# Optimization experiments

Measured on AMD Instinct MI355X. Metric: run time of the kernel, lower is better.

Reference implementation:

```python
import jax, jax.numpy as jnp
import numpy as np

WINDOW_SIZE = 11
SIGMA = 1.5
C1 = 0.01 ** 2
C2 = 0.03 ** 2


def _gaussian_window(window_size=WINDOW_SIZE, sigma=SIGMA):
    coords = jnp.arange(window_size, dtype=jnp.float32) - window_size // 2
    g = jnp.exp(-(coords ** 2) / (2.0 * sigma ** 2))
    g = g / g.sum()
    w3d = g[:, None, None] * g[None, :, None] * g[None, None, :]
    w3d = w3d / w3d.sum()
    return w3d[None, None]  # [1, 1, K, K, K] (OIDHW)


def _gconv3d(x, window):
    # depthwise 3D conv, SAME padding (pad = K//2), groups = C
    C = x.shape[1]
    w = jnp.broadcast_to(window, (C, 1) + window.shape[2:])
    pad = window.shape[-1] // 2
    return jax.lax.conv_general_dilated(
        x, w,
        window_strides=(1, 1, 1),
        padding=[(pad, pad)] * 3,
        dimension_numbers=("NCDHW", "OIDHW", "NCDHW"),
        feature_group_count=C,
    )


def setup_inputs() -> dict:
    key = jax.random.key(0)
    k1, k2 = jax.random.split(key)
    shape = (4, 1, 64, 192, 192)  # [B, C, D, H, W]
    pred = jax.random.uniform(k1, shape, dtype=jnp.float32)
    target = jax.random.uniform(k2, shape, dtype=jnp.float32)
    return {"pred": pred, "target": target}


def reference(pred, target):
    window = _gaussian_window()
    mu_p = _gconv3d(pred, window)
    mu_t = _gconv3d(target, window)
    mu_p_sq = mu_p ** 2
    mu_t_sq = mu_t ** 2
    mu_pt = mu_p * mu_t
    sigma_p_sq = _gconv3d(pred ** 2, window) - mu_p_sq
    sigma_t_sq = _gconv3d(target ** 2, window) - mu_t_sq
    sigma_pt = _gconv3d(pred * target, window) - mu_pt
    ssim_map = ((2.0 * mu_pt + C1) * (2.0 * sigma_pt + C2)) / (
        (mu_p_sq + mu_t_sq + C1) * (sigma_p_sq + sigma_t_sq + C2)
    )
    return 1.0 - ssim_map.mean()
```

## Files before the change

### kernel.cpp

```cpp
#include <hip/hip_runtime.h>


#define D_DIM 64
#define H_DIM 192
#define W_DIM 192
#define SLICE (H_DIM * W_DIM)
#define VOL   (D_DIM * SLICE)
#define NB    4
#define KS    11
#define RAD   5
#define TH    32
#define TW    48
#define HT    (TH + 2 * RAD)
#define WTT   (TW + 2 * RAD)
#define SPITCH 59
#define IP2   48
#define IPF2  (HT * IP2)
#define C1F   (0.01f * 0.01f)
#define C2F   (0.03f * 0.03f)

typedef _Float16 h2v __attribute__((ext_vector_type(2)));

__device__ __forceinline__ void make_window(float* g) {
    float s = 0.f;
#pragma unroll
    for (int i = 0; i < KS; ++i) {
        float c = (float)(i - RAD);
        g[i] = expf(-(c * c) * (1.0f / 4.5f));
        s += g[i];
    }
    float inv = 1.0f / s;
#pragma unroll
    for (int i = 0; i < KS; ++i) g[i] *= inv;
}

__global__ __launch_bounds__(256) void hw_blur_kernel(
    const float* __restrict__ pred, const float* __restrict__ targ,
    uint2* __restrict__ Xg, unsigned short* __restrict__ Yg, int b0) {
    __shared__ union U {
        float stage[2 * HT * SPITCH];
        unsigned short obuf[5 * TH * TW];
    } u;
    __shared__ _Float16 interm2[5 * IPF2];
    float* sp = u.stage;
    float* st = u.stage + HT * SPITCH;

    float g[KS];
    make_window(g);

    const int tid = threadIdx.x;
    const int d    = blockIdx.y;
    const int tile = blockIdx.x;
    const int h0 = (tile >> 2) * TH;
    const int w0 = (tile & 3) * TW;
    const int bl = blockIdx.z;

    const int in_base = (b0 + bl) * VOL + d * SLICE;

    for (int i = tid; i < HT * SPITCH; i += 256) {
        int y = i / SPITCH, x = i - y * SPITCH;
        int gh = h0 + y - RAD, gw = w0 + x - RAD;
        float pv = 0.f, tv = 0.f;
        if (x < WTT && (unsigned)gh < (unsigned)H_DIM && (unsigned)gw < (unsigned)W_DIM) {
            int idx = in_base + gh * W_DIM + gw;
            pv = pred[idx];
            tv = targ[idx];
        }
        sp[i] = pv;
        st[i] = tv;
    }
    __syncthreads();

    if (tid < 252) {
        const int y = tid / 6;
        const int x0 = (tid % 6) * 8;
        float wp[18], wt[18];
#pragma unroll
        for (int k = 0; k < 18; ++k) {
            wp[k] = sp[y * SPITCH + x0 + k];
            wt[k] = st[y * SPITCH + x0 + k];
        }
#pragma unroll
        for (int o = 0; o < 8; ++o) {
            float s0 = 0.f, s1 = 0.f, s2 = 0.f, s3 = 0.f, s4 = 0.f;
#pragma unroll
            for (int k = 0; k < KS; ++k) {
                float pv = wp[o + k], tv = wt[o + k], gk = g[k];
                s0 += gk * pv;
                s1 += gk * tv;
                s2 += gk * pv * pv;
                s3 += gk * tv * tv;
                s4 += gk * pv * tv;
            }
            int idx = y * IP2 + x0 + o;
            interm2[0 * IPF2 + idx] = (_Float16)s0;
            interm2[1 * IPF2 + idx] = (_Float16)s1;
            interm2[2 * IPF2 + idx] = (_Float16)s2;
            interm2[3 * IPF2 + idx] = (_Float16)s3;
            interm2[4 * IPF2 + idx] = (_Float16)s4;
        }
    }
    __syncthreads();

    if (tid < 240) {
        const int f = tid / TW;
        const int x = tid % TW;
        const _Float16* col = interm2 + f * IPF2 + x;
        unsigned short* ob = u.obuf + f * (TH * TW) + x;
        float acc[KS];
#pragma unroll
        for (int s = 0; s < KS; ++s) acc[s] = 0.f;
#pragma unroll
        for (int yy = 0; yy < HT; ++yy) {
            float v = (float)col[yy * IP2];
#pragma unroll
            for (int m = 0; m < KS; ++m) {
                if (yy < 10 && m < 10 - yy) continue;
                acc[(yy + m + 1) % KS] += g[10 - m] * v;
            }
            if (yy >= 10) {
                const int y = yy - 10;
                const int s = (yy + 1) % KS;
                _Float16 h = (_Float16)acc[s];
                ob[y * TW] = *(unsigned short*)&h;
                acc[s] = 0.f;
            }
        }
    }
    __syncthreads();

    const size_t pl_base = (size_t)(bl * D_DIM + d) * SLICE;
#pragma unroll
    for (int it = 0; it < 6; ++it) {
        int px = it * 256 + tid;
        int y = px / TW, x = px - y * TW;
        unsigned a0 = u.obuf[0 * (TH * TW) + px];
        unsigned a1 = u.obuf[1 * (TH * TW) + px];
        unsigned a2 = u.obuf[2 * (TH * TW) + px];
        unsigned a3 = u.obuf[3 * (TH * TW) + px];
        unsigned a4 = u.obuf[4 * (TH * TW) + px];
        size_t gi = pl_base + (size_t)(h0 + y) * W_DIM + (w0 + x);
        Xg[gi] = make_uint2(a0 | (a1 << 16), a2 | (a3 << 16));
        Yg[gi] = (unsigned short)a4;
    }
}


#define LOADP(s, q) do {                                                  \
    const int _o = (q) * SLICE;                                           \
    uint2 _r = xg[_o];                                                    \
    h2v _l = __builtin_bit_cast(h2v, _r.x);                               \
    h2v _h = __builtin_bit_cast(h2v, _r.y);                               \
    w0[s] = (float)_l[0]; w1[s] = (float)_l[1];                           \
    w2[s] = (float)_h[0]; w3[s] = (float)_h[1];                           \
    w4[s] = (float)__builtin_bit_cast(_Float16, (unsigned short)yg[(q) * SLICE]); \
} while (0)

#define PRE(i, q) do {                                                    \
    xr##i = xg[(q) * SLICE];                                              \
    yr##i = yg[(q) * SLICE];                                              \
} while (0)

#define CMT(s, i) do {                                                    \
    h2v _l = __builtin_bit_cast(h2v, xr##i.x);                            \
    h2v _h = __builtin_bit_cast(h2v, xr##i.y);                            \
    w0[s] = (float)_l[0]; w1[s] = (float)_l[1];                           \
    w2[s] = (float)_h[0]; w3[s] = (float)_h[1];                           \
    w4[s] = (float)__builtin_bit_cast(_Float16, (unsigned short)yr##i);   \
} while (0)

#define SSIM_ACC(MP, MT, E2, T2, PT) do {                                 \
    float _mps = (MP) * (MP), _mts = (MT) * (MT), _mpt = (MP) * (MT);     \
    float _num = (2.f * _mpt + C1F) * (2.f * ((PT) - _mpt) + C2F);        \
    float _den = (_mps + _mts + C1F) *                                    \
                 (((E2) - _mps) + ((T2) - _mts) + C2F);                   \
    ssim_sum += _num * __builtin_amdgcn_rcpf(_den);                       \
} while (0)

#define EMIT_W(r, JHI) do {                                               \
    float _mp = 0.f, _mt = 0.f, _e2 = 0.f, _t2 = 0.f, _pt = 0.f;          \
    _Pragma("unroll")                                                     \
    for (int _j = 0; _j <= (JHI); ++_j) {                                 \
        const int _s = (1 + (r) + _j) % 11; const float _g = g[_j];       \
        _mp += _g * w0[_s]; _mt += _g * w1[_s]; _e2 += _g * w2[_s];       \
        _t2 += _g * w3[_s]; _pt += _g * w4[_s];                           \
    }                                                                     \
    SSIM_ACC(_mp, _mt, _e2, _t2, _pt);                                    \
} while (0)

#define EMIT_IN(d) do {                                                   \
    float _mp = 0.f, _mt = 0.f, _e2 = 0.f, _t2 = 0.f, _pt = 0.f;          \
    _Pragma("unroll")                                                     \
    for (int _j = 5 - (d); _j < 11; ++_j) {                               \
        const int _s = (d) - 5 + _j; const float _g = g[_j];              \
        _mp += _g * w0[_s]; _mt += _g * w1[_s]; _e2 += _g * w2[_s];       \
        _t2 += _g * w3[_s]; _pt += _g * w4[_s];                           \
    }                                                                     \
    SSIM_ACC(_mp, _mt, _e2, _t2, _pt);                                    \
} while (0)

#define RND(r, i, qn)  do { CMT(r, i); PRE(i, qn); EMIT_W(r, 10); } while (0)
#define RNDL(r, i)     do { CMT(r, i); EMIT_W(r, 10); } while (0)

__global__ __launch_bounds__(256) void dblur_ssim_kernel(
    const uint2* __restrict__ Xg, const unsigned short* __restrict__ Yg,
    float* __restrict__ partials) {
    float g[KS];
    make_window(g);

    const int tid = threadIdx.x;
    const int bl = blockIdx.x / 144;
    const int hw = (blockIdx.x % 144) * 256 + tid;
    const int cb = bl * VOL + hw;
    const uint2* xg = Xg + cb;
    const unsigned short* yg = Yg + cb;

    float w0[KS], w1[KS], w2[KS], w3[KS], w4[KS];
    uint2 xr0, xr1, xr2, xr3;
    unsigned yr0, yr1, yr2, yr3;
    float ssim_sum = 0.f;

    if (blockIdx.y == 0) {
        LOADP(0, 0); LOADP(1, 1); LOADP(2, 2); LOADP(3, 3); LOADP(4, 4);
        LOADP(5, 5); LOADP(6, 6); LOADP(7, 7); LOADP(8, 8); LOADP(9, 9);
        LOADP(10, 10);
        PRE(3, 11); PRE(0, 12); PRE(1, 13); PRE(2, 14);
        EMIT_IN(0); EMIT_IN(1); EMIT_IN(2); EMIT_IN(3); EMIT_IN(4); EMIT_IN(5);
        RND(0, 3, 15);  RND(1, 0, 16);  RND(2, 1, 17);  RND(3, 2, 18);
        RND(4, 3, 19);  RND(5, 0, 20);  RND(6, 1, 21);  RND(7, 2, 22);
        RND(8, 3, 23);  RND(9, 0, 24);  RND(10, 1, 25); RND(0, 2, 26);
        RND(1, 3, 27);  RND(2, 0, 28);  RND(3, 1, 29);  RND(4, 2, 30);
        RND(5, 3, 31);  RND(6, 0, 32);  RND(7, 1, 33);  RND(8, 2, 34);
        RND(9, 3, 35);  RND(10, 0, 36);
        RNDL(0, 1); RNDL(1, 2); RNDL(2, 3); RNDL(3, 0);
    } else {
        LOADP(5, 27); LOADP(6, 28); LOADP(7, 29); LOADP(8, 30); LOADP(9, 31);
        LOADP(10, 32); LOADP(0, 33); LOADP(1, 34); LOADP(2, 35); LOADP(3, 36);
        LOADP(4, 37);
        PRE(2, 38); PRE(3, 39); PRE(0, 40); PRE(1, 41);
        EMIT_W(4, 10);
        RND(5, 2, 42);  RND(6, 3, 43);  RND(7, 0, 44);  RND(8, 1, 45);
        RND(9, 2, 46);  RND(10, 3, 47); RND(0, 0, 48);  RND(1, 1, 49);
        RND(2, 2, 50);  RND(3, 3, 51);  RND(4, 0, 52);  RND(5, 1, 53);
        RND(6, 2, 54);  RND(7, 3, 55);  RND(8, 0, 56);  RND(9, 1, 57);
        RND(10, 2, 58); RND(0, 3, 59);  RND(1, 0, 60);  RND(2, 1, 61);
        RND(3, 2, 62);  RND(4, 3, 63);
        RNDL(5, 0); RNDL(6, 1); RNDL(7, 2); RNDL(8, 3);
        EMIT_W(9, 9); EMIT_W(10, 8); EMIT_W(11, 7); EMIT_W(12, 6); EMIT_W(13, 5);
    }

    float a = ssim_sum;
#pragma unroll
    for (int off = 32; off > 0; off >>= 1) a += __shfl_down(a, off, 64);
    __shared__ float red[4];
    int lane = tid & 63, wv = tid >> 6;
    if (lane == 0) red[wv] = a;
    __syncthreads();
    if (tid == 0)
        partials[blockIdx.y * gridDim.x + blockIdx.x] =
            red[0] + red[1] + red[2] + red[3];
}

__global__ __launch_bounds__(256) void finalize_kernel(
    const float* __restrict__ partials, int n, float* __restrict__ out) {
    double a = 0.0;
    for (int i = threadIdx.x; i < n; i += 256) a += (double)partials[i];
#pragma unroll
    for (int off = 32; off > 0; off >>= 1) a += __shfl_down(a, off, 64);
    __shared__ double red[4];
    int lane = threadIdx.x & 63, wv = threadIdx.x >> 6;
    if (lane == 0) red[wv] = a;
    __syncthreads();
    if (threadIdx.x == 0) {
        double s = red[0] + red[1] + red[2] + red[3];
        out[0] = (float)(1.0 - s / (double)((long long)NB * VOL));
    }
}

extern "C" void kernel_launch(void* const* d_in, const int* in_sizes, int n_in,
                              void* d_out, int out_size, void* d_ws, size_t ws_size,
                              hipStream_t stream) {
    const float* pred = (const float*)d_in[0];
    const float* targ = (const float*)d_in[1];
    float* out = (float*)d_out;

    int G = 4;
    while (G > 1 && (size_t)G * VOL * 10 + 8192 > ws_size) G >>= 1;

    uint2* Xg = (uint2*)d_ws;
    unsigned short* Yg = (unsigned short*)((char*)d_ws + (size_t)G * VOL * 8);
    float* partials = (float*)((char*)d_ws + (size_t)G * VOL * 10);
    const int bpc = G * 144;
    const int nchunks = NB / G;

    for (int c = 0; c < nchunks; ++c) {
        hw_blur_kernel<<<dim3(24, D_DIM, G), 256, 0, stream>>>(
            pred, targ, Xg, Yg, c * G);
        dblur_ssim_kernel<<<dim3(bpc, 2), 256, 0, stream>>>(
            Xg, Yg, partials + c * 2 * bpc);
    }
    finalize_kernel<<<1, 256, 0, stream>>>(partials, NB * 288, out);
}
```

Before: 212.9 us.

## Fuse HW and depth blur into single streaming SSIM kernel

Replaces the two-kernel pipeline, which wrote five fp16 blurred planes to global workspace and read them back, with one kernel. Each block owns a 16x16 HW tile and marches through depth, blurring each slice in LDS and accumulating the depth blur in rolling register accumulators. It prefetches the next slice into registers while the current one is computed. This removes the large intermediate global write and read, at the cost of halo re-reads, per-slice barriers and higher register pressure.

```diff
diff --git a/kernel.cpp b/kernel.cpp
--- a/kernel.cpp
+++ b/kernel.cpp
@@ -9,13 +9,10 @@
 #define NB    4
 #define KS    11
 #define RAD   5
-#define TH    32
-#define TW    48
-#define HT    (TH + 2 * RAD)
-#define WTT   (TW + 2 * RAD)
-#define SPITCH 59
-#define IP2   48
-#define IPF2  (HT * IP2)
+#define TIL   16
+#define HLO   26
+#define SP    48
+#define IPX   6
 #define C1F   (0.01f * 0.01f)
 #define C2F   (0.03f * 0.03f)
 
@@ -33,141 +30,6 @@
 #pragma unroll
     for (int i = 0; i < KS; ++i) g[i] *= inv;
 }
-
-__global__ __launch_bounds__(256) void hw_blur_kernel(
-    const float* __restrict__ pred, const float* __restrict__ targ,
-    uint2* __restrict__ Xg, unsigned short* __restrict__ Yg, int b0) {
-    __shared__ union U {
-        float stage[2 * HT * SPITCH];
-        unsigned short obuf[5 * TH * TW];
-    } u;
-    __shared__ _Float16 interm2[5 * IPF2];
-    float* sp = u.stage;
-    float* st = u.stage + HT * SPITCH;
-
-    float g[KS];
-    make_window(g);
-
-    const int tid = threadIdx.x;
-    const int d    = blockIdx.y;
-    const int tile = blockIdx.x;
-    const int h0 = (tile >> 2) * TH;
-    const int w0 = (tile & 3) * TW;
-    const int bl = blockIdx.z;
-
-    const int in_base = (b0 + bl) * VOL + d * SLICE;
-
-    for (int i = tid; i < HT * SPITCH; i += 256) {
-        int y = i / SPITCH, x = i - y * SPITCH;
-        int gh = h0 + y - RAD, gw = w0 + x - RAD;
-        float pv = 0.f, tv = 0.f;
-        if (x < WTT && (unsigned)gh < (unsigned)H_DIM && (unsigned)gw < (unsigned)W_DIM) {
-            int idx = in_base + gh * W_DIM + gw;
-            pv = pred[idx];
-            tv = targ[idx];
-        }
-        sp[i] = pv;
-        st[i] = tv;
-    }
-    __syncthreads();
-
-    if (tid < 252) {
-        const int y = tid / 6;
-        const int x0 = (tid % 6) * 8;
-        float wp[18], wt[18];
-#pragma unroll
-        for (int k = 0; k < 18; ++k) {
-            wp[k] = sp[y * SPITCH + x0 + k];
-            wt[k] = st[y * SPITCH + x0 + k];
-        }
-#pragma unroll
-        for (int o = 0; o < 8; ++o) {
-            float s0 = 0.f, s1 = 0.f, s2 = 0.f, s3 = 0.f, s4 = 0.f;
-#pragma unroll
-            for (int k = 0; k < KS; ++k) {
-                float pv = wp[o + k], tv = wt[o + k], gk = g[k];
-                s0 += gk * pv;
-                s1 += gk * tv;
-                s2 += gk * pv * pv;
-                s3 += gk * tv * tv;
-                s4 += gk * pv * tv;
-            }
-            int idx = y * IP2 + x0 + o;
-            interm2[0 * IPF2 + idx] = (_Float16)s0;
-            interm2[1 * IPF2 + idx] = (_Float16)s1;
-            interm2[2 * IPF2 + idx] = (_Float16)s2;
-            interm2[3 * IPF2 + idx] = (_Float16)s3;
-            interm2[4 * IPF2 + idx] = (_Float16)s4;
-        }
-    }
-    __syncthreads();
-
-    if (tid < 240) {
-        const int f = tid / TW;
-        const int x = tid % TW;
-        const _Float16* col = interm2 + f * IPF2 + x;
-        unsigned short* ob = u.obuf + f * (TH * TW) + x;
-        float acc[KS];
-#pragma unroll
-        for (int s = 0; s < KS; ++s) acc[s] = 0.f;
-#pragma unroll
-        for (int yy = 0; yy < HT; ++yy) {
-            float v = (float)col[yy * IP2];
-#pragma unroll
-            for (int m = 0; m < KS; ++m) {
-                if (yy < 10 && m < 10 - yy) continue;
-                acc[(yy + m + 1) % KS] += g[10 - m] * v;
-            }
-            if (yy >= 10) {
-                const int y = yy - 10;
-                const int s = (yy + 1) % KS;
-                _Float16 h = (_Float16)acc[s];
-                ob[y * TW] = *(unsigned short*)&h;
-                acc[s] = 0.f;
-            }
-        }
-    }
-    __syncthreads();
-
-    const size_t pl_base = (size_t)(bl * D_DIM + d) * SLICE;
-#pragma unroll
-    for (int it = 0; it < 6; ++it) {
-        int px = it * 256 + tid;
-        int y = px / TW, x = px - y * TW;
-        unsigned a0 = u.obuf[0 * (TH * TW) + px];
-        unsigned a1 = u.obuf[1 * (TH * TW) + px];
-        unsigned a2 = u.obuf[2 * (TH * TW) + px];
-        unsigned a3 = u.obuf[3 * (TH * TW) + px];
-        unsigned a4 = u.obuf[4 * (TH * TW) + px];
-        size_t gi = pl_base + (size_t)(h0 + y) * W_DIM + (w0 + x);
-        Xg[gi] = make_uint2(a0 | (a1 << 16), a2 | (a3 << 16));
-        Yg[gi] = (unsigned short)a4;
-    }
-}
-
-
-#define LOADP(s, q) do {                                                  \
-    const int _o = (q) * SLICE;                                           \
-    uint2 _r = xg[_o];                                                    \
-    h2v _l = __builtin_bit_cast(h2v, _r.x);                               \
-    h2v _h = __builtin_bit_cast(h2v, _r.y);                               \
-    w0[s] = (float)_l[0]; w1[s] = (float)_l[1];                           \
-    w2[s] = (float)_h[0]; w3[s] = (float)_h[1];                           \
-    w4[s] = (float)__builtin_bit_cast(_Float16, (unsigned short)yg[(q) * SLICE]); \
-} while (0)
-
-#define PRE(i, q) do {                                                    \
-    xr##i = xg[(q) * SLICE];                                              \
-    yr##i = yg[(q) * SLICE];                                              \
-} while (0)
-
-#define CMT(s, i) do {                                                    \
-    h2v _l = __builtin_bit_cast(h2v, xr##i.x);                            \
-    h2v _h = __builtin_bit_cast(h2v, xr##i.y);                            \
-    w0[s] = (float)_l[0]; w1[s] = (float)_l[1];                           \
-    w2[s] = (float)_h[0]; w3[s] = (float)_h[1];                           \
-    w4[s] = (float)__builtin_bit_cast(_Float16, (unsigned short)yr##i);   \
-} while (0)
 
 #define SSIM_ACC(MP, MT, E2, T2, PT) do {                                 \
     float _mps = (MP) * (MP), _mts = (MT) * (MT), _mpt = (MP) * (MT);     \
@@ -177,87 +39,152 @@
     ssim_sum += _num * __builtin_amdgcn_rcpf(_den);                       \
 } while (0)
 
-#define EMIT_W(r, JHI) do {                                               \
-    float _mp = 0.f, _mt = 0.f, _e2 = 0.f, _t2 = 0.f, _pt = 0.f;          \
-    _Pragma("unroll")                                                     \
-    for (int _j = 0; _j <= (JHI); ++_j) {                                 \
-        const int _s = (1 + (r) + _j) % 11; const float _g = g[_j];       \
-        _mp += _g * w0[_s]; _mt += _g * w1[_s]; _e2 += _g * w2[_s];       \
-        _t2 += _g * w3[_s]; _pt += _g * w4[_s];                           \
-    }                                                                     \
-    SSIM_ACC(_mp, _mt, _e2, _t2, _pt);                                    \
-} while (0)
-
-#define EMIT_IN(d) do {                                                   \
-    float _mp = 0.f, _mt = 0.f, _e2 = 0.f, _t2 = 0.f, _pt = 0.f;          \
-    _Pragma("unroll")                                                     \
-    for (int _j = 5 - (d); _j < 11; ++_j) {                               \
-        const int _s = (d) - 5 + _j; const float _g = g[_j];              \
-        _mp += _g * w0[_s]; _mt += _g * w1[_s]; _e2 += _g * w2[_s];       \
-        _t2 += _g * w3[_s]; _pt += _g * w4[_s];                           \
-    }                                                                     \
-    SSIM_ACC(_mp, _mt, _e2, _t2, _pt);                                    \
-} while (0)
-
-#define RND(r, i, qn)  do { CMT(r, i); PRE(i, qn); EMIT_W(r, 10); } while (0)
-#define RNDL(r, i)     do { CMT(r, i); EMIT_W(r, 10); } while (0)
-
-__global__ __launch_bounds__(256) void dblur_ssim_kernel(
-    const uint2* __restrict__ Xg, const unsigned short* __restrict__ Yg,
+__global__ __launch_bounds__(256) void fused_ssim_kernel(
+    const float* __restrict__ pred, const float* __restrict__ targ,
     float* __restrict__ partials) {
+    __shared__ float spb[HLO * SP];
+    __shared__ float stb[HLO * SP];
+    __shared__ __attribute__((aligned(16))) _Float16 interm[HLO * TIL * IPX];
+    __shared__ float red[4];
+
     float g[KS];
     make_window(g);
 
     const int tid = threadIdx.x;
-    const int bl = blockIdx.x / 144;
-    const int hw = (blockIdx.x % 144) * 256 + tid;
-    const int cb = bl * VOL + hw;
-    const uint2* xg = Xg + cb;
-    const unsigned short* yg = Yg + cb;
-
-    float w0[KS], w1[KS], w2[KS], w3[KS], w4[KS];
-    uint2 xr0, xr1, xr2, xr3;
-    unsigned yr0, yr1, yr2, yr3;
+    const int h0 = (blockIdx.x / 12) * TIL;
+    const int w0 = (blockIdx.x % 12) * TIL;
+    const int half = blockIdx.y;
+    const float* pb = pred + (size_t)blockIdx.z * VOL;
+    const float* tb = targ + (size_t)blockIdx.z * VOL;
+    const int q0 = half ? 27 : 0;
+    const int q1 = half ? 63 : 36;
+    const int d_lo = half ? 32 : 0;
+    const int d_hi = half ? 63 : 31;
+
+    int sidx[3], slds[3];
+    bool sa[3], sv[3];
+#pragma unroll
+    for (int k = 0; k < 3; ++k) {
+        int i = tid + 256 * k;
+        sa[k] = i < HLO * HLO;
+        int y = i / HLO, x = i - y * HLO;
+        int gh = h0 + y - RAD, gw = w0 + x - RAD;
+        sv[k] = sa[k] && (unsigned)gh < (unsigned)H_DIM &&
+                (unsigned)gw < (unsigned)W_DIM;
+        sidx[k] = gh * W_DIM + gw;
+        slds[k] = y * SP + x;
+    }
+    const int py = tid >> 4, px = tid & 15;
+
+    float a0[KS], a1[KS], a2[KS], a3[KS], a4[KS];
+#pragma unroll
+    for (int j = 0; j < KS; ++j)
+        a0[j] = a1[j] = a2[j] = a3[j] = a4[j] = 0.f;
     float ssim_sum = 0.f;
 
-    if (blockIdx.y == 0) {
-        LOADP(0, 0); LOADP(1, 1); LOADP(2, 2); LOADP(3, 3); LOADP(4, 4);
-        LOADP(5, 5); LOADP(6, 6); LOADP(7, 7); LOADP(8, 8); LOADP(9, 9);
-        LOADP(10, 10);
-        PRE(3, 11); PRE(0, 12); PRE(1, 13); PRE(2, 14);
-        EMIT_IN(0); EMIT_IN(1); EMIT_IN(2); EMIT_IN(3); EMIT_IN(4); EMIT_IN(5);
-        RND(0, 3, 15);  RND(1, 0, 16);  RND(2, 1, 17);  RND(3, 2, 18);
-        RND(4, 3, 19);  RND(5, 0, 20);  RND(6, 1, 21);  RND(7, 2, 22);
-        RND(8, 3, 23);  RND(9, 0, 24);  RND(10, 1, 25); RND(0, 2, 26);
-        RND(1, 3, 27);  RND(2, 0, 28);  RND(3, 1, 29);  RND(4, 2, 30);
-        RND(5, 3, 31);  RND(6, 0, 32);  RND(7, 1, 33);  RND(8, 2, 34);
-        RND(9, 3, 35);  RND(10, 0, 36);
-        RNDL(0, 1); RNDL(1, 2); RNDL(2, 3); RNDL(3, 0);
-    } else {
-        LOADP(5, 27); LOADP(6, 28); LOADP(7, 29); LOADP(8, 30); LOADP(9, 31);
-        LOADP(10, 32); LOADP(0, 33); LOADP(1, 34); LOADP(2, 35); LOADP(3, 36);
-        LOADP(4, 37);
-        PRE(2, 38); PRE(3, 39); PRE(0, 40); PRE(1, 41);
-        EMIT_W(4, 10);
-        RND(5, 2, 42);  RND(6, 3, 43);  RND(7, 0, 44);  RND(8, 1, 45);
-        RND(9, 2, 46);  RND(10, 3, 47); RND(0, 0, 48);  RND(1, 1, 49);
-        RND(2, 2, 50);  RND(3, 3, 51);  RND(4, 0, 52);  RND(5, 1, 53);
-        RND(6, 2, 54);  RND(7, 3, 55);  RND(8, 0, 56);  RND(9, 1, 57);
-        RND(10, 2, 58); RND(0, 3, 59);  RND(1, 0, 60);  RND(2, 1, 61);
-        RND(3, 2, 62);  RND(4, 3, 63);
-        RNDL(5, 0); RNDL(6, 1); RNDL(7, 2); RNDL(8, 3);
-        EMIT_W(9, 9); EMIT_W(10, 8); EMIT_W(11, 7); EMIT_W(12, 6); EMIT_W(13, 5);
+    float rp[3], rt[3];
+    {
+        const float* pq = pb + q0 * SLICE;
+        const float* tq = tb + q0 * SLICE;
+#pragma unroll
+        for (int k = 0; k < 3; ++k) {
+            rp[k] = sv[k] ? pq[sidx[k]] : 0.f;
+            rt[k] = sv[k] ? tq[sidx[k]] : 0.f;
+        }
+    }
+
+    for (int q = q0;; ++q) {
+        __syncthreads();
+#pragma unroll
+        for (int k = 0; k < 3; ++k)
+            if (sa[k]) { spb[slds[k]] = rp[k]; stb[slds[k]] = rt[k]; }
+        if (q < q1) {
+            const float* pn = pb + (q + 1) * SLICE;
+            const float* tn = tb + (q + 1) * SLICE;
+#pragma unroll
+            for (int k = 0; k < 3; ++k) {
+                rp[k] = sv[k] ? pn[sidx[k]] : 0.f;
+                rt[k] = sv[k] ? tn[sidx[k]] : 0.f;
+            }
+        }
+        __syncthreads();
+
+#pragma unroll
+        for (int it = 0; it < 2; ++it) {
+            int t = tid + it * 256;
+            if (t < HLO * TIL) {
+                int r = t >> 4, c = t & 15;
+                const float* pr = spb + r * SP + c;
+                const float* tr = stb + r * SP + c;
+                float s0 = 0.f, s1 = 0.f, s2 = 0.f, s3 = 0.f, s4 = 0.f;
+#pragma unroll
+                for (int k = 0; k < KS; ++k) {
+                    float pv = pr[k], tv = tr[k], gk = g[k];
+                    s0 += gk * pv;
+                    s1 += gk * tv;
+                    s2 += gk * pv * pv;
+                    s3 += gk * tv * tv;
+                    s4 += gk * pv * tv;
+                }
+                _Float16* ip = interm + t * IPX;
+                h2v w01, w23;
+                w01[0] = (_Float16)s0; w01[1] = (_Float16)s1;
+                w23[0] = (_Float16)s2; w23[1] = (_Float16)s3;
+                *(h2v*)ip = w01;
+                *(h2v*)(ip + 2) = w23;
+                ip[4] = (_Float16)s4;
+            }
+        }
+        __syncthreads();
+
+        {
+            const _Float16* cb = interm + px * IPX;
+            float v0 = 0.f, v1 = 0.f, v2 = 0.f, v3 = 0.f, v4 = 0.f;
+#pragma unroll
+            for (int k = 0; k < KS; ++k) {
+                const _Float16* p = cb + (py + k) * (TIL * IPX);
+                h2v w01 = *(const h2v*)p;
+                h2v w23 = *(const h2v*)(p + 2);
+                float gk = g[k];
+                v0 += gk * (float)w01[0];
+                v1 += gk * (float)w01[1];
+                v2 += gk * (float)w23[0];
+                v3 += gk * (float)w23[1];
+                v4 += gk * (float)p[4];
+            }
+#pragma unroll
+            for (int j = 0; j < KS; ++j) {
+                float wj = g[10 - j];
+                a0[j] += wj * v0; a1[j] += wj * v1; a2[j] += wj * v2;
+                a3[j] += wj * v3; a4[j] += wj * v4;
+            }
+            if (q - 5 >= d_lo)
+                SSIM_ACC(a0[0], a1[0], a2[0], a3[0], a4[0]);
+#pragma unroll
+            for (int j = 0; j < KS - 1; ++j) {
+                a0[j] = a0[j + 1]; a1[j] = a1[j + 1]; a2[j] = a2[j + 1];
+                a3[j] = a3[j + 1]; a4[j] = a4[j + 1];
+            }
+            a0[10] = 0.f; a1[10] = 0.f; a2[10] = 0.f; a3[10] = 0.f; a4[10] = 0.f;
+        }
+        if (q == q1) break;
+    }
+
+#pragma unroll
+    for (int j = 0; j < 5; ++j) {
+        int d = q1 - 4 + j;
+        if (d >= d_lo && d <= d_hi)
+            SSIM_ACC(a0[j], a1[j], a2[j], a3[j], a4[j]);
     }
 
     float a = ssim_sum;
 #pragma unroll
     for (int off = 32; off > 0; off >>= 1) a += __shfl_down(a, off, 64);
-    __shared__ float red[4];
     int lane = tid & 63, wv = tid >> 6;
     if (lane == 0) red[wv] = a;
     __syncthreads();
     if (tid == 0)
-        partials[blockIdx.y * gridDim.x + blockIdx.x] =
+        partials[((blockIdx.z * 2 + blockIdx.y) * 144) + blockIdx.x] =
             red[0] + red[1] + red[2] + red[3];
 }
 
@@ -283,21 +210,8 @@
     const float* pred = (const float*)d_in[0];
     const float* targ = (const float*)d_in[1];
     float* out = (float*)d_out;
-
-    int G = 4;
-    while (G > 1 && (size_t)G * VOL * 10 + 8192 > ws_size) G >>= 1;
-
-    uint2* Xg = (uint2*)d_ws;
-    unsigned short* Yg = (unsigned short*)((char*)d_ws + (size_t)G * VOL * 8);
-    float* partials = (float*)((char*)d_ws + (size_t)G * VOL * 10);
-    const int bpc = G * 144;
-    const int nchunks = NB / G;
-
-    for (int c = 0; c < nchunks; ++c) {
-        hw_blur_kernel<<<dim3(24, D_DIM, G), 256, 0, stream>>>(
-            pred, targ, Xg, Yg, c * G);
-        dblur_ssim_kernel<<<dim3(bpc, 2), 256, 0, stream>>>(
-            Xg, Yg, partials + c * 2 * bpc);
-    }
+    float* partials = (float*)d_ws;
+
+    fused_ssim_kernel<<<dim3(144, 2, NB), 256, 0, stream>>>(pred, targ, partials);
     finalize_kernel<<<1, 256, 0, stream>>>(partials, NB * 288, out);
 }
```

Result: slower. 225.8 us (+6.1%).
